# Kernel optimization log

Measured on AMD Instinct MI355X. Metric: run time of the kernel, lower is better.

Reference implementation:

```python
import jax, jax.numpy as jnp
import numpy as np

N = 50000   # nodes
E = 800000  # edges (avg degree 16)
H = 256     # hidden_dim
OUT = 256   # out_dim


def _leaky(x, slope=0.01):
    return jnp.where(x >= 0, x, slope * x)


def _mlp3(x, W1, b1, W2, b2, W3, b3):
    # MLP(hidden, hidden/2, hidden/2, hidden) with LeakyReLU(0.01) between layers
    x = _leaky(x @ W1 + b1)
    x = _leaky(x @ W2 + b2)
    return x @ W3 + b3


def setup_inputs() -> dict:
    key = jax.random.key(0)
    ks = jax.random.split(key, 16)
    Hh = H // 2

    def w(k, i, o):
        return (jax.random.normal(k, (i, o), jnp.float32) / np.float32(np.sqrt(i)))

    return {
        'h': jax.random.normal(ks[0], (N, H), jnp.float32),
        'src': jax.random.randint(ks[1], (E,), 0, N, dtype=jnp.int32),
        'dst': jax.random.randint(ks[2], (E,), 0, N, dtype=jnp.int32),
        'r': jax.random.randint(ks[3], (E,), 0, 2, dtype=jnp.int32),
        'inv': jax.random.randint(ks[4], (N,), 0, 2, dtype=jnp.int32),
        'inv_W1': w(ks[5], H, Hh), 'inv_b1': jnp.zeros((Hh,), jnp.float32),
        'inv_W2': w(ks[6], Hh, Hh), 'inv_b2': jnp.zeros((Hh,), jnp.float32),
        'inv_W3': w(ks[7], Hh, H), 'inv_b3': jnp.zeros((H,), jnp.float32),
        'and_W1': w(ks[8], H, Hh), 'and_b1': jnp.zeros((Hh,), jnp.float32),
        'and_W2': w(ks[9], Hh, Hh), 'and_b2': jnp.zeros((Hh,), jnp.float32),
        'and_W3': w(ks[10], Hh, H), 'and_b3': jnp.zeros((H,), jnp.float32),
        'proj_W1': w(ks[11], H, H), 'proj_b1': jnp.zeros((H,), jnp.float32),
        'proj_W2': w(ks[12], H, OUT), 'proj_b2': jnp.zeros((OUT,), jnp.float32),
    }


def reference(h, src, dst, r, inv,
              inv_W1, inv_b1, inv_W2, inv_b2, inv_W3, inv_b3,
              and_W1, and_b1, and_W2, and_b2, and_W3, and_b3,
              proj_W1, proj_b1, proj_W2, proj_b2):
    # edge_msg: gather src features, apply func_inv on edges with r == 1
    msg = h[src]  # [E, H]
    msg = jnp.where((r == 1)[:, None],
                    _mlp3(msg, inv_W1, inv_b1, inv_W2, inv_b2, inv_W3, inv_b3),
                    msg)
    # fn.mean('m', 'neigh'): mean over incoming edges per destination node
    sums = jax.ops.segment_sum(msg, dst, num_segments=N)          # [N, H]
    cnt = jax.ops.segment_sum(jnp.ones((E,), msg.dtype), dst, num_segments=N)
    neigh = sums / jnp.maximum(cnt, 1.0)[:, None]
    # apply_nodes_func: func_and, then func_inv where inv flag set
    res = _mlp3(neigh, and_W1, and_b1, and_W2, and_b2, and_W3, and_b3)
    res = jnp.where((inv == 1)[:, None],
                    _mlp3(res, inv_W1, inv_b1, inv_W2, inv_b2, inv_W3, inv_b3),
                    res)
    # proj_head: MLP(H, H, OUT) with negative_slope=0 (i.e. ReLU)
    out = jax.nn.relu(res @ proj_W1 + proj_b1) @ proj_W2 + proj_b2
    return out
```

## Files before the change

### kernel.cpp

```cpp
#include <hip/hip_runtime.h>

typedef __bf16 bf16_t;
typedef _Float16 f16_t;
typedef f16_t f16x2 __attribute__((ext_vector_type(2)));
typedef f16_t f16x4 __attribute__((ext_vector_type(4)));
typedef bf16_t bf16x2 __attribute__((ext_vector_type(2)));
typedef bf16_t bf16x4 __attribute__((ext_vector_type(4)));
typedef bf16_t bf16x8 __attribute__((ext_vector_type(8)));
typedef float f32x4 __attribute__((ext_vector_type(4)));
typedef float f32x16 __attribute__((ext_vector_type(16)));

#define MFMA16(a, b, c) __builtin_amdgcn_mfma_f32_16x16x32_bf16(a, b, c, 0, 0, 0)
#define MFMA32(a, b, c) __builtin_amdgcn_mfma_f32_32x32x16_bf16(a, b, c, 0, 0, 0)

__device__ __forceinline__ float leaky01(float v) { return v >= 0.f ? v : 0.01f * v; }

__device__ __forceinline__ void acc_f16x4(float& s0, float& s1, float& s2, float& s3,
                                          f16x4 v)
{
#if __has_builtin(__builtin_amdgcn_fdot2)
    const f16x2 K10 = (f16x2){(f16_t)1.0f, (f16_t)0.0f};
    const f16x2 K01 = (f16x2){(f16_t)0.0f, (f16_t)1.0f};
    f16x2 lo = (f16x2){v.x, v.y};
    f16x2 hi = (f16x2){v.z, v.w};
    s0 = __builtin_amdgcn_fdot2(lo, K10, s0, false);
    s1 = __builtin_amdgcn_fdot2(lo, K01, s1, false);
    s2 = __builtin_amdgcn_fdot2(hi, K10, s2, false);
    s3 = __builtin_amdgcn_fdot2(hi, K01, s3, false);
#else
    s0 += (float)v.x; s1 += (float)v.y; s2 += (float)v.z; s3 += (float)v.w;
#endif
}

#define OFF_IW1 0
#define OFF_IW2 65536
#define OFF_IW3 98304
#define OFF_AW1 163840
#define OFF_AW2 229376
#define OFF_AW3 262144
#define OFF_PW1 327680
#define OFF_PW2 458752
#define OFF_M3  589824
#define WP_TOTAL 622592

template<int KD, int NC, int NCT>
__device__ __forceinline__ void gemm_tile(
    const bf16_t* __restrict__ ah, const bf16_t* __restrict__ al, int sa,
    const bf16_t* __restrict__ Bh, const bf16_t* __restrict__ Bl,
    int cb, int qd, int ln, f32x4 (&acc)[2][4])
{
#pragma unroll
    for (int rt = 0; rt < 2; ++rt)
#pragma unroll
        for (int ct = 0; ct < NCT; ++ct) acc[rt][ct] = (f32x4){0.f, 0.f, 0.f, 0.f};
#pragma unroll
    for (int k0 = 0; k0 < KD; k0 += 32) {
        int ka = k0 + qd * 8;
        bf16x8 a0h = *(const bf16x8*)&ah[ln * sa + ka];
        bf16x8 a1h = *(const bf16x8*)&ah[(16 + ln) * sa + ka];
        bf16x8 a0l = *(const bf16x8*)&al[ln * sa + ka];
        bf16x8 a1l = *(const bf16x8*)&al[(16 + ln) * sa + ka];
#pragma unroll
        for (int ct = 0; ct < NCT; ++ct) {
            size_t bo = ((size_t)((k0 >> 5) * 4 + qd) * NC + cb + ct * 16 + ln) * 8;
            bf16x8 bh = *(const bf16x8*)(Bh + bo);
            bf16x8 bl = *(const bf16x8*)(Bl + bo);
            acc[0][ct] = MFMA16(a0h, bh, acc[0][ct]);
            acc[0][ct] = MFMA16(a0l, bh, acc[0][ct]);
            acc[0][ct] = MFMA16(a0h, bl, acc[0][ct]);
            acc[1][ct] = MFMA16(a1h, bh, acc[1][ct]);
            acc[1][ct] = MFMA16(a1l, bh, acc[1][ct]);
            acc[1][ct] = MFMA16(a1h, bl, acc[1][ct]);
        }
    }
}

template<int KD, int NC>
__device__ __forceinline__ void gemm32_tile(
    const bf16_t* __restrict__ ah, const bf16_t* __restrict__ al, int sa,
    const bf16_t* __restrict__ Bh, const bf16_t* __restrict__ Bl,
    int cb, int l31, int kh, f32x16 &acc)
{
    f32x16 c0, c1;
#pragma unroll
    for (int i = 0; i < 16; ++i) { c0[i] = 0.f; c1[i] = 0.f; }
    const int arow = l31 * sa + kh * 8;
    const int bcol = cb + l31;
#pragma unroll
    for (int kc = 0; kc < KD; kc += 32) {
        bf16x8 ah0 = *(const bf16x8*)&ah[arow + kc];
        bf16x8 al0 = *(const bf16x8*)&al[arow + kc];
        bf16x8 ah1 = *(const bf16x8*)&ah[arow + kc + 16];
        bf16x8 al1 = *(const bf16x8*)&al[arow + kc + 16];
        size_t bo0 = ((size_t)((kc >> 3) + kh) * NC + bcol) * 8;
        size_t bo1 = ((size_t)((kc >> 3) + 2 + kh) * NC + bcol) * 8;
        bf16x8 bh0 = *(const bf16x8*)(Bh + bo0);
        bf16x8 bl0 = *(const bf16x8*)(Bl + bo0);
        bf16x8 bh1 = *(const bf16x8*)(Bh + bo1);
        bf16x8 bl1 = *(const bf16x8*)(Bl + bo1);
        c0 = MFMA32(ah0, bh0, c0);
        c1 = MFMA32(ah1, bh1, c1);
        c0 = MFMA32(al0, bh0, c0);
        c1 = MFMA32(al1, bh1, c1);
        c0 = MFMA32(ah0, bl0, c0);
        c1 = MFMA32(ah1, bl1, c1);
    }
    acc = c0 + c1;
}

template<int NCT>
__device__ __forceinline__ void epi_split(
    f32x4 (&acc)[2][4], const float* __restrict__ bias,
    int cb, int qd, int ln, bf16_t* dh, bf16_t* dl, int stride, int act)
{
#pragma unroll
    for (int ct = 0; ct < NCT; ++ct) {
        int col = cb + ct * 16 + ln;
        float bb = bias ? bias[col] : 0.f;
#pragma unroll
        for (int rt = 0; rt < 2; ++rt)
#pragma unroll
            for (int r = 0; r < 4; ++r) {
                float v = acc[rt][ct][r] + bb;
                if (act == 1) v = leaky01(v);
                else if (act == 2) v = fmaxf(v, 0.f);
                int row = rt * 16 + qd * 4 + r;
                bf16_t h = (bf16_t)v;
                dh[row * stride + col] = h;
                dl[row * stride + col] = (bf16_t)(v - (float)h);
            }
    }
}

template<int ACT>
__device__ __forceinline__ void epi32_split(
    const f32x16 &acc, const float* __restrict__ bias,
    int cb, int l31, int kh, bf16_t* dh, bf16_t* dl, int stride)
{
    int col = cb + l31;
    float bb = bias[col];
#pragma unroll
    for (int r = 0; r < 16; ++r) {
        float v = acc[r] + bb;
        if (ACT == 1) v = leaky01(v);
        else if (ACT == 2) v = fmaxf(v, 0.f);
        int row = (r & 3) + 8 * (r >> 2) + 4 * kh;
        bf16_t h = (bf16_t)v;
        dh[row * stride + col] = h;
        dl[row * stride + col] = (bf16_t)(v - (float)h);
    }
}

__global__ __launch_bounds__(512, 4) void kernelA(
    const float* __restrict__ h, f16_t* __restrict__ zbuf,
    const bf16_t* __restrict__ wp, const float* __restrict__ ib1,
    const float* __restrict__ ib2, const float* __restrict__ c3f, int M,
    int tiles, const int* __restrict__ dstE, int* __restrict__ cnt, int E)
{
    __shared__ bf16_t Xh[32][264], Xl[32][264];
    __shared__ bf16_t Yh[32][136], Yl[32][136];

    const int tid = threadIdx.x;

    if ((int)blockIdx.x >= tiles) {
        int e = (blockIdx.x - tiles) * 512 + tid;
        if (e < E) atomicAdd(&cnt[dstE[e]], 1);
        return;
    }

    const int row0 = blockIdx.x * 32;
    const int lane = tid & 63;
    const int wv = tid >> 6;
    const int qd = lane >> 4;
    const int ln = lane & 15;
    const int cb = wv * 16;
    const int l31 = lane & 31;
    const int kh = lane >> 5;

    {
        const float4* src4 = (const float4*)(h + (size_t)row0 * 256);
#pragma unroll
        for (int i = 0; i < 4; ++i) {
            int q = i * 512 + tid;
            int row = q >> 6;
            int kc = (q & 63) * 4;
            float4 v = make_float4(0.f, 0.f, 0.f, 0.f);
            if (row0 + row < M) v = src4[q];
            bf16_t h0 = (bf16_t)v.x; bf16_t l0 = (bf16_t)(v.x - (float)h0);
            bf16_t h1 = (bf16_t)v.y; bf16_t l1 = (bf16_t)(v.y - (float)h1);
            bf16_t h2 = (bf16_t)v.z; bf16_t l2 = (bf16_t)(v.z - (float)h2);
            bf16_t h3 = (bf16_t)v.w; bf16_t l3 = (bf16_t)(v.w - (float)h3);
            *(bf16x4*)&Xh[row][kc] = (bf16x4){h0, h1, h2, h3};
            *(bf16x4*)&Xl[row][kc] = (bf16x4){l0, l1, l2, l3};
        }
    }
    __syncthreads();

    {
        const bool isz = wv < 4;
        const int cb32 = (wv & 3) * 32;
        const bf16_t* Bh = wp + (isz ? OFF_AW1 : OFF_IW1);
        f32x16 a32;
        gemm32_tile<256, 128>(&Xh[0][0], &Xl[0][0], 264, Bh, Bh + 32768,
                              cb32, l31, kh, a32);
        int col = cb32 + l31;
        if (isz) {
#pragma unroll
            for (int r = 0; r < 16; ++r) {
                int lrow = (r & 3) + 8 * (r >> 2) + 4 * kh;
                int row = row0 + lrow;
                if (row < M) zbuf[((size_t)row * 2) * 128 + col] = (f16_t)a32[r];
            }
        } else {
            float bb = ib1[col];
#pragma unroll
            for (int r = 0; r < 16; ++r) {
                int lrow = (r & 3) + 8 * (r >> 2) + 4 * kh;
                float v = leaky01(a32[r] + bb);
                bf16_t hh = (bf16_t)v;
                Yh[lrow][col] = hh;
                Yl[lrow][col] = (bf16_t)(v - (float)hh);
            }
        }
    }
    __syncthreads();

    f32x4 acc[2][4];

    gemm_tile<128, 128, 1>(&Yh[0][0], &Yl[0][0], 136, wp + OFF_IW2, wp + OFF_IW2 + 16384, cb, qd, ln, acc);
    epi_split<1>(acc, ib2, cb, qd, ln, &Xh[0][0], &Xl[0][0], 264, 1);
    __syncthreads();

    gemm_tile<128, 128, 1>(&Xh[0][0], &Xl[0][0], 264, wp + OFF_M3, wp + OFF_M3 + 16384, cb, qd, ln, acc);
    {
        int col = cb + ln;
        float bb = c3f[col];
#pragma unroll
        for (int rt = 0; rt < 2; ++rt)
#pragma unroll
            for (int r = 0; r < 4; ++r) {
                int row = row0 + rt * 16 + qd * 4 + r;
                if (row < M) zbuf[((size_t)row * 2 + 1) * 128 + col] = (f16_t)(acc[rt][0][r] + bb);
            }
    }
}

__global__ __launch_bounds__(512, 4) void kernelB(
    const f16_t* __restrict__ zbuf, const int* __restrict__ ridx,
    const int* __restrict__ offs, const int* __restrict__ cnt,
    const float* __restrict__ ab1, const int* __restrict__ invf,
    float* __restrict__ out, const bf16_t* __restrict__ wp,
    const float* __restrict__ ab2, const float* __restrict__ ab3,
    const float* __restrict__ ib1, const float* __restrict__ ib2,
    const float* __restrict__ ib3, const float* __restrict__ pb1,
    const float* __restrict__ pb2, int M)
{
    __shared__ bf16_t Ch[32][264], Cl[32][264];
    __shared__ bf16_t Ah[32][136], Al[32][136];
    __shared__ int sflag[32];

    const int tid = threadIdx.x;
    const int row0 = blockIdx.x * 32;
    const int lane = tid & 63;
    const int wv = tid >> 6;
    const int qd = lane >> 4;
    const int ln = lane & 15;
    const int cb2 = wv * 16;
    const int l31 = lane & 31;
    const int kh = lane >> 5;
    const int cb32 = wv * 32;

    const int hw = tid >> 5;
    const int hl = tid & 31;
    const int hbase = lane & 32;
    const f16x4* zp4 = (const f16x4*)zbuf;

#pragma unroll
    for (int pass = 0; pass < 2; ++pass) {
        int nl = pass * 16 + hw;
        int row = row0 + nl;
        float s0 = 0.f, s1 = 0.f, s2 = 0.f, s3 = 0.f;
        int c = 0;
        if (row < M) {
            int beg = offs[row];
            c = cnt[row];
            for (int base = 0; base < c; base += 32) {
                int rem = c - base; if (rem > 32) rem = 32;
                int myr = (hl < rem) ? ridx[beg + base + hl] : 0;
                int j = 0;
                for (; j + 16 <= rem; j += 16) {
                    f16x4 v[16];
#pragma unroll
                    for (int i = 0; i < 16; ++i) {
                        int rr = __shfl(myr, hbase + j + i);
                        v[i] = zp4[(size_t)rr * 32 + hl];
                    }
#pragma unroll
                    for (int i = 0; i < 16; ++i)
                        acc_f16x4(s0, s1, s2, s3, v[i]);
                }
                for (; j + 8 <= rem; j += 8) {
                    f16x4 v[8];
#pragma unroll
                    for (int i = 0; i < 8; ++i) {
                        int rr = __shfl(myr, hbase + j + i);
                        v[i] = zp4[(size_t)rr * 32 + hl];
                    }
#pragma unroll
                    for (int i = 0; i < 8; ++i)
                        acc_f16x4(s0, s1, s2, s3, v[i]);
                }
                for (; j < rem; ++j) {
                    int rr = __shfl(myr, hbase + j);
                    f16x4 vv = zp4[(size_t)rr * 32 + hl];
                    acc_f16x4(s0, s1, s2, s3, vv);
                }
            }
        }
        float invc = 1.0f / fmaxf((float)c, 1.0f);
        float4 bv = *(const float4*)&ab1[hl * 4];
        float m0 = leaky01(s0 * invc + bv.x);
        float m1 = leaky01(s1 * invc + bv.y);
        float m2 = leaky01(s2 * invc + bv.z);
        float m3 = leaky01(s3 * invc + bv.w);
        bf16_t h0 = (bf16_t)m0; bf16_t l0 = (bf16_t)(m0 - (float)h0);
        bf16_t h1 = (bf16_t)m1; bf16_t l1 = (bf16_t)(m1 - (float)h1);
        bf16_t h2 = (bf16_t)m2; bf16_t l2 = (bf16_t)(m2 - (float)h2);
        bf16_t h3 = (bf16_t)m3; bf16_t l3 = (bf16_t)(m3 - (float)h3);
        *(bf16x4*)&Ah[nl][hl * 4] = (bf16x4){h0, h1, h2, h3};
        *(bf16x4*)&Al[nl][hl * 4] = (bf16x4){l0, l1, l2, l3};
    }
    if (tid < 32) {
        int rr = row0 + tid;
        sflag[tid] = (rr < M) ? invf[rr] : 0;
    }
    __syncthreads();

    f32x4 acc[2][4];
    f32x16 c32;

    gemm_tile<128, 128, 1>(&Ah[0][0], &Al[0][0], 136, wp + OFF_AW2, wp + OFF_AW2 + 16384, cb2, qd, ln, acc);
    __syncthreads();
    epi_split<1>(acc, ab2, cb2, qd, ln, &Ah[0][0], &Al[0][0], 136, 1);
    __syncthreads();

    gemm32_tile<128, 256>(&Ah[0][0], &Al[0][0], 136, wp + OFF_AW3, wp + OFF_AW3 + 32768, cb32, l31, kh, c32);
    epi32_split<0>(c32, ab3, cb32, l31, kh, &Ch[0][0], &Cl[0][0], 264);
    __syncthreads();

    gemm_tile<256, 128, 1>(&Ch[0][0], &Cl[0][0], 264, wp + OFF_IW1, wp + OFF_IW1 + 32768, cb2, qd, ln, acc);
    epi_split<1>(acc, ib1, cb2, qd, ln, &Ah[0][0], &Al[0][0], 136, 1);
    __syncthreads();

    gemm_tile<128, 128, 1>(&Ah[0][0], &Al[0][0], 136, wp + OFF_IW2, wp + OFF_IW2 + 16384, cb2, qd, ln, acc);
    __syncthreads();
    epi_split<1>(acc, ib2, cb2, qd, ln, &Ah[0][0], &Al[0][0], 136, 1);
    __syncthreads();

    gemm32_tile<128, 256>(&Ah[0][0], &Al[0][0], 136, wp + OFF_IW3, wp + OFF_IW3 + 32768, cb32, l31, kh, c32);
    {
        int col = cb32 + l31;
        float bb = ib3[col];
#pragma unroll
        for (int r = 0; r < 16; ++r) {
            int row = (r & 3) + 8 * (r >> 2) + 4 * kh;
            if (sflag[row] == 1) {
                float v = c32[r] + bb;
                bf16_t hh = (bf16_t)v;
                Ch[row][col] = hh;
                Cl[row][col] = (bf16_t)(v - (float)hh);
            }
        }
    }
    __syncthreads();

    gemm32_tile<256, 256>(&Ch[0][0], &Cl[0][0], 264, wp + OFF_PW1, wp + OFF_PW1 + 65536, cb32, l31, kh, c32);
    __syncthreads();
    epi32_split<2>(c32, pb1, cb32, l31, kh, &Ch[0][0], &Cl[0][0], 264);
    __syncthreads();

    gemm32_tile<256, 256>(&Ch[0][0], &Cl[0][0], 264, wp + OFF_PW2, wp + OFF_PW2 + 65536, cb32, l31, kh, c32);
    {
        int col = cb32 + l31;
        float bb = pb2[col];
#pragma unroll
        for (int r = 0; r < 16; ++r) {
            int lrow = (r & 3) + 8 * (r >> 2) + 4 * kh;
            int row = row0 + lrow;
            if (row < M) out[(size_t)row * 256 + col] = c32[r] + bb;
        }
    }
}

__global__ void mc3_kernel(const float* __restrict__ iW3, const float* __restrict__ aW1,
                           const float* __restrict__ ib3, float* __restrict__ m3f,
                           float* __restrict__ c3f)
{
    int b = blockIdx.x;
    if (b < 64) {
        int idx = b * 256 + threadIdx.x;
        int k = idx >> 7, j = idx & 127;
        float s = 0.f;
        for (int t = 0; t < 256; ++t) s += iW3[k * 256 + t] * aW1[t * 128 + j];
        m3f[idx] = s;
    } else {
        int j = threadIdx.x;
        if (j < 128) {
            float s = 0.f;
            for (int t = 0; t < 256; ++t) s += ib3[t] * aW1[t * 128 + j];
            c3f[j] = s;
        }
    }
}

__global__ void pack_all(const float* s0, const float* s1, const float* s2,
                         const float* s3, const float* s4, const float* s5,
                         const float* s6, const float* s7, const float* s8,
                         bf16_t* dst)
{
    const float* srcs[9] = {s0, s1, s2, s3, s4, s5, s6, s7, s8};
    const int lgN[9] = {7, 7, 8, 7, 7, 8, 8, 8, 7};
    const int sz[9]  = {32768, 16384, 32768, 32768, 16384, 32768, 65536, 65536, 16384};
    const int off[9] = {OFF_IW1, OFF_IW2, OFF_IW3, OFF_AW1, OFF_AW2, OFF_AW3,
                        OFF_PW1, OFF_PW2, OFF_M3};
    int m = blockIdx.y;
    int idx = blockIdx.x * blockDim.x + threadIdx.x;
    if (idx >= sz[m]) return;
    int lg = lgN[m];
    int Nc = 1 << lg;
    int k = idx >> lg;
    int n = idx & (Nc - 1);
    float w = srcs[m][idx];
    bf16_t hi = (bf16_t)w;
    bf16_t lo = (bf16_t)(w - (float)hi);
    int p = (((k >> 5) * 4 + ((k >> 3) & 3)) * Nc + n) * 8 + (k & 7);
    bf16_t* dh = dst + off[m];
    dh[p] = hi;
    dh[sz[m] + p] = lo;
}

__global__ void scan1(const int* __restrict__ cnt, int* __restrict__ offs,
                      int* __restrict__ bsum, int Nn)
{
    __shared__ int s[256];
    int tid = threadIdx.x;
    int g = blockIdx.x * 256 + tid;
    int v = (g < Nn) ? cnt[g] : 0;
    s[tid] = v;
    __syncthreads();
    for (int off = 1; off < 256; off <<= 1) {
        int u = (tid >= off) ? s[tid - off] : 0;
        __syncthreads();
        s[tid] += u;
        __syncthreads();
    }
    if (g < Nn) offs[g] = s[tid] - v;
    if (tid == 255) bsum[blockIdx.x] = s[255];
}

__global__ void scan2(int* __restrict__ bsum, int NB)
{
    __shared__ int s[256];
    int tid = threadIdx.x;
    if (NB > 256) {
        if (tid == 0) {
            int run = 0;
            for (int i = 0; i < NB; ++i) { int v = bsum[i]; bsum[i] = run; run += v; }
        }
        return;
    }
    int v = (tid < NB) ? bsum[tid] : 0;
    s[tid] = v;
    __syncthreads();
    for (int off = 1; off < 256; off <<= 1) {
        int u = (tid >= off) ? s[tid - off] : 0;
        __syncthreads();
        s[tid] += u;
        __syncthreads();
    }
    if (tid < NB) bsum[tid] = s[tid] - v;
}

__global__ void scan3(int* __restrict__ offs, const int* __restrict__ bsum,
                      int* __restrict__ cursor, int Nn)
{
    int g = blockIdx.x * 256 + threadIdx.x;
    if (g < Nn) {
        int o = offs[g] + bsum[blockIdx.x];
        offs[g] = o;
        cursor[g] = o;
    }
}

__global__ void fill_kernel(const int* __restrict__ dst, const int* __restrict__ src,
                            const int* __restrict__ r, int* __restrict__ cursor,
                            int* __restrict__ ridx, int E)
{
    int e = blockIdx.x * blockDim.x + threadIdx.x;
    if (e < E) {
        int p = atomicAdd(&cursor[dst[e]], 1);
        ridx[p] = src[e] * 2 + r[e];
    }
}

extern "C" void kernel_launch(void* const* d_in, const int* in_sizes, int n_in,
                              void* d_out, int out_size, void* d_ws, size_t ws_size,
                              hipStream_t stream)
{
    const float* h   = (const float*)d_in[0];
    const int* src   = (const int*)d_in[1];
    const int* dst   = (const int*)d_in[2];
    const int* r     = (const int*)d_in[3];
    const int* inv   = (const int*)d_in[4];
    const float* iW1 = (const float*)d_in[5];
    const float* ib1 = (const float*)d_in[6];
    const float* iW2 = (const float*)d_in[7];
    const float* ib2 = (const float*)d_in[8];
    const float* iW3 = (const float*)d_in[9];
    const float* ib3 = (const float*)d_in[10];
    const float* aW1 = (const float*)d_in[11];
    const float* ab1 = (const float*)d_in[12];
    const float* aW2 = (const float*)d_in[13];
    const float* ab2 = (const float*)d_in[14];
    const float* aW3 = (const float*)d_in[15];
    const float* ab3 = (const float*)d_in[16];
    const float* pW1 = (const float*)d_in[17];
    const float* pb1 = (const float*)d_in[18];
    const float* pW2 = (const float*)d_in[19];
    const float* pb2 = (const float*)d_in[20];

    const int N = in_sizes[0] / 256;
    const int E = in_sizes[1];
    float* out = (float*)d_out;

    f16_t* zbuf = (f16_t*)d_ws;
    int* cnt    = (int*)(zbuf + (size_t)2 * N * 128);
    int* offs   = cnt + N;
    int* cursor = offs + N;
    int* bsum   = cursor + N;
    int* ridx   = bsum + 256;
    bf16_t* wp  = (bf16_t*)(ridx + E);
    float* m3f  = (float*)(wp + WP_TOTAL);
    float* c3f  = m3f + 16384;

    (void)hipMemsetAsync(cnt, 0, (size_t)N * sizeof(int), stream);

    mc3_kernel<<<65, 256, 0, stream>>>(iW3, aW1, ib3, m3f, c3f);
    pack_all<<<dim3(256, 9), 256, 0, stream>>>(iW1, iW2, iW3, aW1, aW2, aW3,
                                               pW1, pW2, m3f, wp);

    const int tiles = (N + 31) / 32;
    const int EB = (E + 511) / 512;
    const int NB = (N + 255) / 256;

    kernelA<<<tiles + EB, 512, 0, stream>>>(h, zbuf, wp, ib1, ib2, c3f, N,
                                            tiles, dst, cnt, E);

    scan1<<<NB, 256, 0, stream>>>(cnt, offs, bsum, N);
    scan2<<<1, 256, 0, stream>>>(bsum, NB);
    scan3<<<NB, 256, 0, stream>>>(offs, bsum, cursor, N);
    fill_kernel<<<(E + 255) / 256, 256, 0, stream>>>(dst, src, r, cursor, ridx, E);

    kernelB<<<tiles, 512, 0, stream>>>(zbuf, ridx, offs, cnt, ab1, inv, out, wp,
                                       ab2, ab3, ib1, ib2, ib3, pb1, pb2, N);
}
```

Baseline: 391.4 us.

## Replace split-bf16 triple MFMA with single fp16 MFMA and 64-row tiles

Drops the hi/lo bf16 split emulation of fp32 (three MFMAs per product) and uses plain fp16 operands with one MFMA per tile, halving packed weight storage and shared memory per row. Tiles grow from 32 to 64 rows per block so each weight fragment load is reused across four (or two) row tiles. Accuracy falls to fp16 precision for activations and weights, which risks overflow or tolerance failures, and the larger LDS footprint per block may lower occupancy.

```diff
diff --git a/kernel.cpp b/kernel.cpp
--- a/kernel.cpp
+++ b/kernel.cpp
@@ -1,17 +1,14 @@
 #include <hip/hip_runtime.h>
 
-typedef __bf16 bf16_t;
 typedef _Float16 f16_t;
 typedef f16_t f16x2 __attribute__((ext_vector_type(2)));
 typedef f16_t f16x4 __attribute__((ext_vector_type(4)));
-typedef bf16_t bf16x2 __attribute__((ext_vector_type(2)));
-typedef bf16_t bf16x4 __attribute__((ext_vector_type(4)));
-typedef bf16_t bf16x8 __attribute__((ext_vector_type(8)));
+typedef f16_t f16x8 __attribute__((ext_vector_type(8)));
 typedef float f32x4 __attribute__((ext_vector_type(4)));
 typedef float f32x16 __attribute__((ext_vector_type(16)));
 
-#define MFMA16(a, b, c) __builtin_amdgcn_mfma_f32_16x16x32_bf16(a, b, c, 0, 0, 0)
-#define MFMA32(a, b, c) __builtin_amdgcn_mfma_f32_32x32x16_bf16(a, b, c, 0, 0, 0)
+#define MFMA16H(a, b, c) __builtin_amdgcn_mfma_f32_16x16x32_f16(a, b, c, 0, 0, 0)
+#define MFMA32H(a, b, c) __builtin_amdgcn_mfma_f32_32x32x16_f16(a, b, c, 0, 0, 0)
 
 __device__ __forceinline__ float leaky01(float v) { return v >= 0.f ? v : 0.01f * v; }
 
@@ -33,132 +30,110 @@
 }
 
 #define OFF_IW1 0
-#define OFF_IW2 65536
-#define OFF_IW3 98304
-#define OFF_AW1 163840
-#define OFF_AW2 229376
-#define OFF_AW3 262144
-#define OFF_PW1 327680
-#define OFF_PW2 458752
-#define OFF_M3  589824
-#define WP_TOTAL 622592
-
-template<int KD, int NC, int NCT>
-__device__ __forceinline__ void gemm_tile(
-    const bf16_t* __restrict__ ah, const bf16_t* __restrict__ al, int sa,
-    const bf16_t* __restrict__ Bh, const bf16_t* __restrict__ Bl,
-    int cb, int qd, int ln, f32x4 (&acc)[2][4])
-{
-#pragma unroll
-    for (int rt = 0; rt < 2; ++rt)
-#pragma unroll
-        for (int ct = 0; ct < NCT; ++ct) acc[rt][ct] = (f32x4){0.f, 0.f, 0.f, 0.f};
+#define OFF_IW2 32768
+#define OFF_IW3 49152
+#define OFF_AW1 81920
+#define OFF_AW2 114688
+#define OFF_AW3 131072
+#define OFF_PW1 163840
+#define OFF_PW2 229376
+#define OFF_M3  294912
+#define WP_TOTAL 311296
+
+template<int KD, int NC>
+__device__ __forceinline__ void gemm16(
+    const f16_t* __restrict__ a, int sa, const f16_t* __restrict__ B,
+    int cb, int qd, int ln, f32x4 (&acc)[4])
+{
+#pragma unroll
+    for (int rt = 0; rt < 4; ++rt) acc[rt] = (f32x4){0.f, 0.f, 0.f, 0.f};
 #pragma unroll
     for (int k0 = 0; k0 < KD; k0 += 32) {
         int ka = k0 + qd * 8;
-        bf16x8 a0h = *(const bf16x8*)&ah[ln * sa + ka];
-        bf16x8 a1h = *(const bf16x8*)&ah[(16 + ln) * sa + ka];
-        bf16x8 a0l = *(const bf16x8*)&al[ln * sa + ka];
-        bf16x8 a1l = *(const bf16x8*)&al[(16 + ln) * sa + ka];
-#pragma unroll
-        for (int ct = 0; ct < NCT; ++ct) {
-            size_t bo = ((size_t)((k0 >> 5) * 4 + qd) * NC + cb + ct * 16 + ln) * 8;
-            bf16x8 bh = *(const bf16x8*)(Bh + bo);
-            bf16x8 bl = *(const bf16x8*)(Bl + bo);
-            acc[0][ct] = MFMA16(a0h, bh, acc[0][ct]);
-            acc[0][ct] = MFMA16(a0l, bh, acc[0][ct]);
-            acc[0][ct] = MFMA16(a0h, bl, acc[0][ct]);
-            acc[1][ct] = MFMA16(a1h, bh, acc[1][ct]);
-            acc[1][ct] = MFMA16(a1l, bh, acc[1][ct]);
-            acc[1][ct] = MFMA16(a1h, bl, acc[1][ct]);
-        }
+        f16x8 b = *(const f16x8*)(B + ((size_t)((k0 >> 5) * 4 + qd) * NC + cb + ln) * 8);
+        f16x8 a0 = *(const f16x8*)&a[ln * sa + ka];
+        f16x8 a1 = *(const f16x8*)&a[(16 + ln) * sa + ka];
+        f16x8 a2 = *(const f16x8*)&a[(32 + ln) * sa + ka];
+        f16x8 a3 = *(const f16x8*)&a[(48 + ln) * sa + ka];
+        acc[0] = MFMA16H(a0, b, acc[0]);
+        acc[1] = MFMA16H(a1, b, acc[1]);
+        acc[2] = MFMA16H(a2, b, acc[2]);
+        acc[3] = MFMA16H(a3, b, acc[3]);
     }
 }
 
 template<int KD, int NC>
-__device__ __forceinline__ void gemm32_tile(
-    const bf16_t* __restrict__ ah, const bf16_t* __restrict__ al, int sa,
-    const bf16_t* __restrict__ Bh, const bf16_t* __restrict__ Bl,
-    int cb, int l31, int kh, f32x16 &acc)
+__device__ __forceinline__ void gemm32(
+    const f16_t* __restrict__ a, int sa, const f16_t* __restrict__ B,
+    int cb, int l31, int kh, f32x16 &o0, f32x16 &o1)
 {
     f32x16 c0, c1;
 #pragma unroll
     for (int i = 0; i < 16; ++i) { c0[i] = 0.f; c1[i] = 0.f; }
-    const int arow = l31 * sa + kh * 8;
+    const int ar0 = l31 * sa + kh * 8;
+    const int ar1 = (32 + l31) * sa + kh * 8;
     const int bcol = cb + l31;
 #pragma unroll
     for (int kc = 0; kc < KD; kc += 32) {
-        bf16x8 ah0 = *(const bf16x8*)&ah[arow + kc];
-        bf16x8 al0 = *(const bf16x8*)&al[arow + kc];
-        bf16x8 ah1 = *(const bf16x8*)&ah[arow + kc + 16];
-        bf16x8 al1 = *(const bf16x8*)&al[arow + kc + 16];
-        size_t bo0 = ((size_t)((kc >> 3) + kh) * NC + bcol) * 8;
-        size_t bo1 = ((size_t)((kc >> 3) + 2 + kh) * NC + bcol) * 8;
-        bf16x8 bh0 = *(const bf16x8*)(Bh + bo0);
-        bf16x8 bl0 = *(const bf16x8*)(Bl + bo0);
-        bf16x8 bh1 = *(const bf16x8*)(Bh + bo1);
-        bf16x8 bl1 = *(const bf16x8*)(Bl + bo1);
-        c0 = MFMA32(ah0, bh0, c0);
-        c1 = MFMA32(ah1, bh1, c1);
-        c0 = MFMA32(al0, bh0, c0);
-        c1 = MFMA32(al1, bh1, c1);
-        c0 = MFMA32(ah0, bl0, c0);
-        c1 = MFMA32(ah1, bl1, c1);
-    }
-    acc = c0 + c1;
-}
-
-template<int NCT>
-__device__ __forceinline__ void epi_split(
-    f32x4 (&acc)[2][4], const float* __restrict__ bias,
-    int cb, int qd, int ln, bf16_t* dh, bf16_t* dl, int stride, int act)
-{
-#pragma unroll
-    for (int ct = 0; ct < NCT; ++ct) {
-        int col = cb + ct * 16 + ln;
-        float bb = bias ? bias[col] : 0.f;
-#pragma unroll
-        for (int rt = 0; rt < 2; ++rt)
-#pragma unroll
-            for (int r = 0; r < 4; ++r) {
-                float v = acc[rt][ct][r] + bb;
-                if (act == 1) v = leaky01(v);
-                else if (act == 2) v = fmaxf(v, 0.f);
-                int row = rt * 16 + qd * 4 + r;
-                bf16_t h = (bf16_t)v;
-                dh[row * stride + col] = h;
-                dl[row * stride + col] = (bf16_t)(v - (float)h);
-            }
-    }
+        f16x8 b0 = *(const f16x8*)(B + ((size_t)((kc >> 3) + kh) * NC + bcol) * 8);
+        f16x8 b1 = *(const f16x8*)(B + ((size_t)((kc >> 3) + 2 + kh) * NC + bcol) * 8);
+        f16x8 a00 = *(const f16x8*)&a[ar0 + kc];
+        f16x8 a01 = *(const f16x8*)&a[ar0 + kc + 16];
+        f16x8 a10 = *(const f16x8*)&a[ar1 + kc];
+        f16x8 a11 = *(const f16x8*)&a[ar1 + kc + 16];
+        c0 = MFMA32H(a00, b0, c0);
+        c1 = MFMA32H(a10, b0, c1);
+        c0 = MFMA32H(a01, b1, c0);
+        c1 = MFMA32H(a11, b1, c1);
+    }
+    o0 = c0; o1 = c1;
 }
 
 template<int ACT>
-__device__ __forceinline__ void epi32_split(
-    const f32x16 &acc, const float* __restrict__ bias,
-    int cb, int l31, int kh, bf16_t* dh, bf16_t* dl, int stride)
+__device__ __forceinline__ void epi16(
+    f32x4 (&acc)[4], const float* __restrict__ bias,
+    int cb, int qd, int ln, f16_t* d, int stride)
+{
+    int col = cb + ln;
+    float bb = bias[col];
+#pragma unroll
+    for (int rt = 0; rt < 4; ++rt)
+#pragma unroll
+        for (int r = 0; r < 4; ++r) {
+            float v = acc[rt][r] + bb;
+            if (ACT == 1) v = leaky01(v);
+            else if (ACT == 2) v = fmaxf(v, 0.f);
+            d[(rt * 16 + qd * 4 + r) * stride + col] = (f16_t)v;
+        }
+}
+
+template<int ACT>
+__device__ __forceinline__ void epi32(
+    const f32x16 &a0, const f32x16 &a1, const float* __restrict__ bias,
+    int cb, int l31, int kh, f16_t* d, int stride)
 {
     int col = cb + l31;
     float bb = bias[col];
 #pragma unroll
     for (int r = 0; r < 16; ++r) {
-        float v = acc[r] + bb;
-        if (ACT == 1) v = leaky01(v);
-        else if (ACT == 2) v = fmaxf(v, 0.f);
+        float v0 = a0[r] + bb;
+        float v1 = a1[r] + bb;
+        if (ACT == 1) { v0 = leaky01(v0); v1 = leaky01(v1); }
+        else if (ACT == 2) { v0 = fmaxf(v0, 0.f); v1 = fmaxf(v1, 0.f); }
         int row = (r & 3) + 8 * (r >> 2) + 4 * kh;
-        bf16_t h = (bf16_t)v;
-        dh[row * stride + col] = h;
-        dl[row * stride + col] = (bf16_t)(v - (float)h);
+        d[row * stride + col] = (f16_t)v0;
+        d[(32 + row) * stride + col] = (f16_t)v1;
     }
 }
 
 __global__ __launch_bounds__(512, 4) void kernelA(
     const float* __restrict__ h, f16_t* __restrict__ zbuf,
-    const bf16_t* __restrict__ wp, const float* __restrict__ ib1,
+    const f16_t* __restrict__ wp, const float* __restrict__ ib1,
     const float* __restrict__ ib2, const float* __restrict__ c3f, int M,
     int tiles, const int* __restrict__ dstE, int* __restrict__ cnt, int E)
 {
-    __shared__ bf16_t Xh[32][264], Xl[32][264];
-    __shared__ bf16_t Yh[32][136], Yl[32][136];
+    __shared__ f16_t X[64][264];
+    __shared__ f16_t Y[64][136];
 
     const int tid = threadIdx.x;
 
@@ -168,7 +143,7 @@
         return;
     }
 
-    const int row0 = blockIdx.x * 32;
+    const int row0 = blockIdx.x * 64;
     const int lane = tid & 63;
     const int wv = tid >> 6;
     const int qd = lane >> 4;
@@ -180,18 +155,13 @@
     {
         const float4* src4 = (const float4*)(h + (size_t)row0 * 256);
 #pragma unroll
-        for (int i = 0; i < 4; ++i) {
+        for (int i = 0; i < 8; ++i) {
             int q = i * 512 + tid;
             int row = q >> 6;
             int kc = (q & 63) * 4;
             float4 v = make_float4(0.f, 0.f, 0.f, 0.f);
             if (row0 + row < M) v = src4[q];
-            bf16_t h0 = (bf16_t)v.x; bf16_t l0 = (bf16_t)(v.x - (float)h0);
-            bf16_t h1 = (bf16_t)v.y; bf16_t l1 = (bf16_t)(v.y - (float)h1);
-            bf16_t h2 = (bf16_t)v.z; bf16_t l2 = (bf16_t)(v.z - (float)h2);
-            bf16_t h3 = (bf16_t)v.w; bf16_t l3 = (bf16_t)(v.w - (float)h3);
-            *(bf16x4*)&Xh[row][kc] = (bf16x4){h0, h1, h2, h3};
-            *(bf16x4*)&Xl[row][kc] = (bf16x4){l0, l1, l2, l3};
+            *(f16x4*)&X[row][kc] = (f16x4){(f16_t)v.x, (f16_t)v.y, (f16_t)v.z, (f16_t)v.w};
         }
     }
     __syncthreads();
@@ -199,48 +169,47 @@
     {
         const bool isz = wv < 4;
         const int cb32 = (wv & 3) * 32;
-        const bf16_t* Bh = wp + (isz ? OFF_AW1 : OFF_IW1);
-        f32x16 a32;
-        gemm32_tile<256, 128>(&Xh[0][0], &Xl[0][0], 264, Bh, Bh + 32768,
-                              cb32, l31, kh, a32);
+        const f16_t* Bw = wp + (isz ? OFF_AW1 : OFF_IW1);
+        f32x16 z0, z1;
+        gemm32<256, 128>(&X[0][0], 264, Bw, cb32, l31, kh, z0, z1);
         int col = cb32 + l31;
         if (isz) {
 #pragma unroll
             for (int r = 0; r < 16; ++r) {
                 int lrow = (r & 3) + 8 * (r >> 2) + 4 * kh;
                 int row = row0 + lrow;
-                if (row < M) zbuf[((size_t)row * 2) * 128 + col] = (f16_t)a32[r];
+                if (row < M) zbuf[((size_t)row * 2) * 128 + col] = (f16_t)z0[r];
+                row += 32;
+                if (row < M) zbuf[((size_t)row * 2) * 128 + col] = (f16_t)z1[r];
             }
         } else {
             float bb = ib1[col];
 #pragma unroll
             for (int r = 0; r < 16; ++r) {
                 int lrow = (r & 3) + 8 * (r >> 2) + 4 * kh;
-                float v = leaky01(a32[r] + bb);
-                bf16_t hh = (bf16_t)v;
-                Yh[lrow][col] = hh;
-                Yl[lrow][col] = (bf16_t)(v - (float)hh);
+                Y[lrow][col] = (f16_t)leaky01(z0[r] + bb);
+                Y[32 + lrow][col] = (f16_t)leaky01(z1[r] + bb);
             }
         }
     }
     __syncthreads();
 
-    f32x4 acc[2][4];
-
-    gemm_tile<128, 128, 1>(&Yh[0][0], &Yl[0][0], 136, wp + OFF_IW2, wp + OFF_IW2 + 16384, cb, qd, ln, acc);
-    epi_split<1>(acc, ib2, cb, qd, ln, &Xh[0][0], &Xl[0][0], 264, 1);
-    __syncthreads();
-
-    gemm_tile<128, 128, 1>(&Xh[0][0], &Xl[0][0], 264, wp + OFF_M3, wp + OFF_M3 + 16384, cb, qd, ln, acc);
+    f32x4 a4[4];
+
+    gemm16<128, 128>(&Y[0][0], 136, wp + OFF_IW2, cb, qd, ln, a4);
+    epi16<1>(a4, ib2, cb, qd, ln, &X[0][0], 264);
+    __syncthreads();
+
+    gemm16<128, 128>(&X[0][0], 264, wp + OFF_M3, cb, qd, ln, a4);
     {
         int col = cb + ln;
         float bb = c3f[col];
 #pragma unroll
-        for (int rt = 0; rt < 2; ++rt)
+        for (int rt = 0; rt < 4; ++rt)
 #pragma unroll
             for (int r = 0; r < 4; ++r) {
                 int row = row0 + rt * 16 + qd * 4 + r;
-                if (row < M) zbuf[((size_t)row * 2 + 1) * 128 + col] = (f16_t)(acc[rt][0][r] + bb);
+                if (row < M) zbuf[((size_t)row * 2 + 1) * 128 + col] = (f16_t)(a4[rt][r] + bb);
             }
     }
 }
@@ -249,18 +218,18 @@
     const f16_t* __restrict__ zbuf, const int* __restrict__ ridx,
     const int* __restrict__ offs, const int* __restrict__ cnt,
     const float* __restrict__ ab1, const int* __restrict__ invf,
-    float* __restrict__ out, const bf16_t* __restrict__ wp,
+    float* __restrict__ out, const f16_t* __restrict__ wp,
     const float* __restrict__ ab2, const float* __restrict__ ab3,
     const float* __restrict__ ib1, const float* __restrict__ ib2,
     const float* __restrict__ ib3, const float* __restrict__ pb1,
     const float* __restrict__ pb2, int M)
 {
-    __shared__ bf16_t Ch[32][264], Cl[32][264];
-    __shared__ bf16_t Ah[32][136], Al[32][136];
-    __shared__ int sflag[32];
+    __shared__ f16_t C[64][264];
+    __shared__ f16_t A[64][136];
+    __shared__ int sflag[64];
 
     const int tid = threadIdx.x;
-    const int row0 = blockIdx.x * 32;
+    const int row0 = blockIdx.x * 64;
     const int lane = tid & 63;
     const int wv = tid >> 6;
     const int qd = lane >> 4;
@@ -276,7 +245,7 @@
     const f16x4* zp4 = (const f16x4*)zbuf;
 
 #pragma unroll
-    for (int pass = 0; pass < 2; ++pass) {
+    for (int pass = 0; pass < 4; ++pass) {
         int nl = pass * 16 + hw;
         int row = row0 + nl;
         float s0 = 0.f, s1 = 0.f, s2 = 0.f, s3 = 0.f;
@@ -323,63 +292,54 @@
         float m1 = leaky01(s1 * invc + bv.y);
         float m2 = leaky01(s2 * invc + bv.z);
         float m3 = leaky01(s3 * invc + bv.w);
-        bf16_t h0 = (bf16_t)m0; bf16_t l0 = (bf16_t)(m0 - (float)h0);
-        bf16_t h1 = (bf16_t)m1; bf16_t l1 = (bf16_t)(m1 - (float)h1);
-        bf16_t h2 = (bf16_t)m2; bf16_t l2 = (bf16_t)(m2 - (float)h2);
-        bf16_t h3 = (bf16_t)m3; bf16_t l3 = (bf16_t)(m3 - (float)h3);
-        *(bf16x4*)&Ah[nl][hl * 4] = (bf16x4){h0, h1, h2, h3};
-        *(bf16x4*)&Al[nl][hl * 4] = (bf16x4){l0, l1, l2, l3};
-    }
-    if (tid < 32) {
+        *(f16x4*)&A[nl][hl * 4] = (f16x4){(f16_t)m0, (f16_t)m1, (f16_t)m2, (f16_t)m3};
+    }
+    if (tid < 64) {
         int rr = row0 + tid;
         sflag[tid] = (rr < M) ? invf[rr] : 0;
     }
     __syncthreads();
 
-    f32x4 acc[2][4];
-    f32x16 c32;
-
-    gemm_tile<128, 128, 1>(&Ah[0][0], &Al[0][0], 136, wp + OFF_AW2, wp + OFF_AW2 + 16384, cb2, qd, ln, acc);
-    __syncthreads();
-    epi_split<1>(acc, ab2, cb2, qd, ln, &Ah[0][0], &Al[0][0], 136, 1);
-    __syncthreads();
-
-    gemm32_tile<128, 256>(&Ah[0][0], &Al[0][0], 136, wp + OFF_AW3, wp + OFF_AW3 + 32768, cb32, l31, kh, c32);
-    epi32_split<0>(c32, ab3, cb32, l31, kh, &Ch[0][0], &Cl[0][0], 264);
-    __syncthreads();
-
-    gemm_tile<256, 128, 1>(&Ch[0][0], &Cl[0][0], 264, wp + OFF_IW1, wp + OFF_IW1 + 32768, cb2, qd, ln, acc);
-    epi_split<1>(acc, ib1, cb2, qd, ln, &Ah[0][0], &Al[0][0], 136, 1);
-    __syncthreads();
-
-    gemm_tile<128, 128, 1>(&Ah[0][0], &Al[0][0], 136, wp + OFF_IW2, wp + OFF_IW2 + 16384, cb2, qd, ln, acc);
-    __syncthreads();
-    epi_split<1>(acc, ib2, cb2, qd, ln, &Ah[0][0], &Al[0][0], 136, 1);
-    __syncthreads();
-
-    gemm32_tile<128, 256>(&Ah[0][0], &Al[0][0], 136, wp + OFF_IW3, wp + OFF_IW3 + 32768, cb32, l31, kh, c32);
+    f32x4 a4[4];
+    f32x16 c0, c1;
+
+    gemm16<128, 128>(&A[0][0], 136, wp + OFF_AW2, cb2, qd, ln, a4);
+    __syncthreads();
+    epi16<1>(a4, ab2, cb2, qd, ln, &A[0][0], 136);
+    __syncthreads();
+
+    gemm32<128, 256>(&A[0][0], 136, wp + OFF_AW3, cb32, l31, kh, c0, c1);
+    epi32<0>(c0, c1, ab3, cb32, l31, kh, &C[0][0], 264);
+    __syncthreads();
+
+    gemm16<256, 128>(&C[0][0], 264, wp + OFF_IW1, cb2, qd, ln, a4);
+    epi16<1>(a4, ib1, cb2, qd, ln, &A[0][0], 136);
+    __syncthreads();
+
+    gemm16<128, 128>(&A[0][0], 136, wp + OFF_IW2, cb2, qd, ln, a4);
+    __syncthreads();
+    epi16<1>(a4, ib2, cb2, qd, ln, &A[0][0], 136);
+    __syncthreads();
+
+    gemm32<128, 256>(&A[0][0], 136, wp + OFF_IW3, cb32, l31, kh, c0, c1);
     {
         int col = cb32 + l31;
         float bb = ib3[col];
 #pragma unroll
         for (int r = 0; r < 16; ++r) {
-            int row = (r & 3) + 8 * (r >> 2) + 4 * kh;
-            if (sflag[row] == 1) {
-                float v = c32[r] + bb;
-                bf16_t hh = (bf16_t)v;
-                Ch[row][col] = hh;
-                Cl[row][col] = (bf16_t)(v - (float)hh);
-            }
-        }
-    }
-    __syncthreads();
-
-    gemm32_tile<256, 256>(&Ch[0][0], &Cl[0][0], 264, wp + OFF_PW1, wp + OFF_PW1 + 65536, cb32, l31, kh, c32);
-    __syncthreads();
-    epi32_split<2>(c32, pb1, cb32, l31, kh, &Ch[0][0], &Cl[0][0], 264);
-    __syncthreads();
-
-    gemm32_tile<256, 256>(&Ch[0][0], &Cl[0][0], 264, wp + OFF_PW2, wp + OFF_PW2 + 65536, cb32, l31, kh, c32);
+            int lrow = (r & 3) + 8 * (r >> 2) + 4 * kh;
+            if (sflag[lrow] == 1) C[lrow][col] = (f16_t)(c0[r] + bb);
+            if (sflag[32 + lrow] == 1) C[32 + lrow][col] = (f16_t)(c1[r] + bb);
+        }
+    }
+    __syncthreads();
+
+    gemm32<256, 256>(&C[0][0], 264, wp + OFF_PW1, cb32, l31, kh, c0, c1);
+    __syncthreads();
+    epi32<2>(c0, c1, pb1, cb32, l31, kh, &C[0][0], 264);
+    __syncthreads();
+
+    gemm32<256, 256>(&C[0][0], 264, wp + OFF_PW2, cb32, l31, kh, c0, c1);
     {
         int col = cb32 + l31;
         float bb = pb2[col];
@@ -387,7 +347,9 @@
         for (int r = 0; r < 16; ++r) {
             int lrow = (r & 3) + 8 * (r >> 2) + 4 * kh;
             int row = row0 + lrow;
-            if (row < M) out[(size_t)row * 256 + col] = c32[r] + bb;
+            if (row < M) out[(size_t)row * 256 + col] = c0[r] + bb;
+            row += 32;
+            if (row < M) out[(size_t)row * 256 + col] = c1[r] + bb;
         }
     }
 }
@@ -416,7 +378,7 @@
 __global__ void pack_all(const float* s0, const float* s1, const float* s2,
                          const float* s3, const float* s4, const float* s5,
                          const float* s6, const float* s7, const float* s8,
-                         bf16_t* dst)
+                         f16_t* dst)
 {
     const float* srcs[9] = {s0, s1, s2, s3, s4, s5, s6, s7, s8};
     const int lgN[9] = {7, 7, 8, 7, 7, 8, 8, 8, 7};
@@ -430,13 +392,8 @@
     int Nc = 1 << lg;
     int k = idx >> lg;
     int n = idx & (Nc - 1);
-    float w = srcs[m][idx];
-    bf16_t hi = (bf16_t)w;
-    bf16_t lo = (bf16_t)(w - (float)hi);
-    int p = (((k >> 5) * 4 + ((k >> 3) & 3)) * Nc + n) * 8 + (k & 7);
-    bf16_t* dh = dst + off[m];
-    dh[p] = hi;
-    dh[sz[m] + p] = lo;
+    int p = ((k >> 3) * Nc + n) * 8 + (k & 7);
+    dst[off[m] + p] = (f16_t)srcs[m][idx];
 }
 
 __global__ void scan1(const int* __restrict__ cnt, int* __restrict__ offs,
@@ -539,7 +496,7 @@
     int* cursor = offs + N;
     int* bsum   = cursor + N;
     int* ridx   = bsum + 256;
-    bf16_t* wp  = (bf16_t*)(ridx + E);
+    f16_t* wp   = (f16_t*)(ridx + E);
     float* m3f  = (float*)(wp + WP_TOTAL);
     float* c3f  = m3f + 16384;
 
@@ -549,7 +506,7 @@
     pack_all<<<dim3(256, 9), 256, 0, stream>>>(iW1, iW2, iW3, aW1, aW2, aW3,
                                                pW1, pW2, m3f, wp);
 
-    const int tiles = (N + 31) / 32;
+    const int tiles = (N + 63) / 64;
     const int EB = (E + 511) / 512;
     const int NB = (N + 255) / 256;
 
```

Measured after the change: 339.3 us. 13.3% less time.
